# Kernel optimization log

Hardware: AMD Instinct MI355X
Metric: run time of the kernel (lower is better)

The kernel has to match this reference:

```python
import jax, jax.numpy as jnp
import numpy as np

B, S, D, H, L, M, V = 4, 4096, 512, 8, 6, 2048, 32000
C, NB, NBEF = 64, 64, 1      # chunk_len, n_buckets, n_chunks_before
DH = D // H


def sinusoid_pos_emb(seq_len, dim):
    pos = np.arange(seq_len, dtype=np.float32)[:, None]
    half = dim // 2
    freq = np.exp(np.arange(half, dtype=np.float32) * -(np.log(10000.0) / (half - 1)))
    pe = np.concatenate([np.sin(pos * freq), np.cos(pos * freq)], axis=-1)
    return jnp.asarray(pe, jnp.float32)  # [S, D]

POS = sinusoid_pos_emb(S, D)


def layer_norm(x, s, b):
    m = x.mean(-1, keepdims=True)
    v = ((x - m) ** 2).mean(-1, keepdims=True)
    return (x - m) * jax.lax.rsqrt(v + 1e-6) * s + b


def lsh_attention(x, Wq, Wv, Wo, rot, pad):
    """Shared-QK LSH bucketed chunked attention (Reformer, n_hashes=1, non-causal)."""
    q = jnp.einsum('bsd,dhf->bhsf', x, Wq.reshape(D, H, DH))
    v = jnp.einsum('bsd,dhf->bhsf', x, Wv.reshape(D, H, DH))
    # random-rotation hashing: bucket = argmax over [rot, -rot] projections
    r = jnp.einsum('bhsf,hfr->bhsr', q, rot)            # [B,H,S,NB//2]
    buckets = jnp.argmax(jnp.concatenate([r, -r], -1), -1)  # [B,H,S] in [0,NB)
    # stable sort by (bucket, position)
    st = jnp.argsort(buckets * S + jnp.arange(S), axis=-1)  # [B,H,S]
    g = lambda t: jnp.take_along_axis(t, st[..., None], axis=2)
    sq = g(q)
    sv = g(v)
    sk = sq  # shared QK (qk_length_norm=False)
    spad = jnp.take_along_axis(jnp.broadcast_to(pad[:, None, :], (B, H, S)), st, axis=2)
    nc = S // C
    cq = sq.reshape(B, H, nc, C, DH)
    ck = sk.reshape(B, H, nc, C, DH)
    cv = sv.reshape(B, H, nc, C, DH)
    cp = spad.reshape(B, H, nc, C)
    # look back NBEF chunks (wrap-around, as in trax look_adjacent)
    look = lambda t: jnp.concatenate([t] + [jnp.roll(t, i, axis=2) for i in range(1, NBEF + 1)], axis=3)
    bk, bv, bp = look(ck), look(cv), look(cp)   # keys of length C*(1+NBEF)
    logits = jnp.einsum('bhncf,bhnkf->bhnck', cq, bk) / jnp.sqrt(jnp.float32(DH))
    logits = jnp.where(bp[:, :, :, None, :], logits, -1e9)  # mask padded keys
    w = jax.nn.softmax(logits, axis=-1)
    o = jnp.einsum('bhnck,bhnkf->bhncf', w, bv).reshape(B, H, S, DH)
    # unsort back to original token order
    inv = jnp.argsort(st, axis=-1)
    o = jnp.take_along_axis(o, inv[..., None], axis=2)
    o = o.transpose(0, 2, 1, 3).reshape(B, S, D)
    return o @ Wo


def reference(tokens, emb, rot, ln1_s, ln1_b, Wq, Wv, Wo, ln2_s, ln2_b, W1, b1, W2, b2, lnf_s, lnf_b):
    pad = tokens > 0                     # [B,S] padding mask
    x = emb[tokens] + POS[None, :, :]    # embed + sinusoidal pos enc
    for l in range(L):
        h = layer_norm(x, ln1_s[l], ln1_b[l])
        x = x + lsh_attention(h, Wq[l], Wv[l], Wo[l], rot[l], pad)
        h = layer_norm(x, ln2_s[l], ln2_b[l])
        h = jax.nn.gelu(h @ W1[l] + b1[l]) @ W2[l] + b2[l]
        x = x + h
    return layer_norm(x, lnf_s, lnf_b)


def setup_inputs():
    key = jax.random.key(0)
    ks = jax.random.split(key, 8)
    w02 = lambda k, sh: jax.random.normal(k, sh, jnp.float32) * 0.02
    return dict(
        tokens=jax.random.randint(ks[0], (B, S), 1, V, dtype=jnp.int32),
        emb=jax.random.normal(ks[1], (V, D), jnp.float32),
        rot=jax.random.normal(ks[2], (L, H, DH, NB // 2), jnp.float32),
        ln1_s=jnp.ones((L, D)), ln1_b=jnp.zeros((L, D)),
        Wq=w02(ks[3], (L, D, D)), Wv=w02(ks[4], (L, D, D)), Wo=w02(ks[5], (L, D, D)),
        ln2_s=jnp.ones((L, D)), ln2_b=jnp.zeros((L, D)),
        W1=w02(ks[6], (L, D, M)), b1=jnp.zeros((L, M)),
        W2=w02(ks[7], (L, M, D)), b2=jnp.zeros((L, D)),
        lnf_s=jnp.ones((D,)), lnf_b=jnp.zeros((D,)),
    )
```

## Files before the change

kernel.cpp:

```cpp
#include <hip/hip_runtime.h>

#define B_ 4
#define S_ 4096
#define D_ 512
#define H_ 8
#define L_ 6
#define M_ 2048
#define DH_ 64
#define NC_ 64
#define C_ 64

typedef _Float16 half8 __attribute__((ext_vector_type(8)));
typedef _Float16 half4 __attribute__((ext_vector_type(4)));
typedef float f32x4 __attribute__((ext_vector_type(4)));

typedef const __attribute__((address_space(1))) unsigned int gu32;
typedef __attribute__((address_space(3))) unsigned int lu32;

#define OQ_ 0
#define OV_ 262144
#define OR_ 524288
#define OO_ 655360
#define O1_ 917504
#define O2_ 1966080
#define WTOT_ 3014656

__global__ __launch_bounds__(128) void embed_kernel(const int* __restrict__ tokens,
                                                    const float* __restrict__ emb,
                                                    float* __restrict__ x) {
  int row = blockIdx.x;
  int s = row & (S_ - 1);
  int tok = tokens[row];
  const float4* e = (const float4*)(emb + (size_t)tok * D_);
  float4* xo = (float4*)(x + (size_t)row * D_);
  int t = threadIdx.x;
  float4 ev = e[t];
  int d0 = t * 4;
  const double c64 = -9.210340371976184 / 255.0;
  float pe[4];
#pragma unroll
  for (int j = 0; j < 4; j++) {
    int d = d0 + j;
    int i = (d < 256) ? d : d - 256;
    double freq = exp((double)i * c64);
    double arg = (double)s * freq;
    pe[j] = (d < 256) ? (float)sin(arg) : (float)cos(arg);
  }
  float4 o;
  o.x = ev.x + pe[0];
  o.y = ev.y + pe[1];
  o.z = ev.z + pe[2];
  o.w = ev.w + pe[3];
  xo[t] = o;
}

__device__ __forceinline__ void ln_core(const float* __restrict__ in, int row, int t,
                                        const float* __restrict__ sc,
                                        const float* __restrict__ bi,
                                        float4& o1, float4& o2) {
  const float4* ir = (const float4*)(in + (size_t)row * D_);
  float4 a = ir[t];
  float4 b4 = ir[t + 64];
  float sum = a.x + a.y + a.z + a.w + b4.x + b4.y + b4.z + b4.w;
  float sq  = a.x*a.x + a.y*a.y + a.z*a.z + a.w*a.w
            + b4.x*b4.x + b4.y*b4.y + b4.z*b4.z + b4.w*b4.w;
#pragma unroll
  for (int m = 1; m < 64; m <<= 1) {
    sum += __shfl_xor(sum, m);
    sq  += __shfl_xor(sq, m);
  }
  float mean = sum * (1.0f / 512.0f);
  float var  = sq * (1.0f / 512.0f) - mean * mean;
  float rstd = 1.0f / sqrtf(var + 1e-6f);
  float4 s1 = ((const float4*)sc)[t], s2 = ((const float4*)sc)[t + 64];
  float4 g1 = ((const float4*)bi)[t], g2 = ((const float4*)bi)[t + 64];
  o1.x = (a.x - mean) * rstd * s1.x + g1.x;
  o1.y = (a.y - mean) * rstd * s1.y + g1.y;
  o1.z = (a.z - mean) * rstd * s1.z + g1.z;
  o1.w = (a.w - mean) * rstd * s1.w + g1.w;
  o2.x = (b4.x - mean) * rstd * s2.x + g2.x;
  o2.y = (b4.y - mean) * rstd * s2.y + g2.y;
  o2.z = (b4.z - mean) * rstd * s2.z + g2.z;
  o2.w = (b4.w - mean) * rstd * s2.w + g2.w;
}

__global__ __launch_bounds__(256) void ln_h(const float* __restrict__ in,
                                            _Float16* __restrict__ hi,
                                            _Float16* __restrict__ lo,
                                            const float* __restrict__ sc,
                                            const float* __restrict__ bi) {
  int row = blockIdx.x * 4 + (threadIdx.x >> 6);
  int t = threadIdx.x & 63;
  float4 o1, o2;
  ln_core(in, row, t, sc, bi, o1, o2);
  float v1[4] = {o1.x, o1.y, o1.z, o1.w};
  float v2[4] = {o2.x, o2.y, o2.z, o2.w};
  half4 h1, l1, h2, l2;
#pragma unroll
  for (int j = 0; j < 4; j++) {
    _Float16 h = (_Float16)v1[j];
    h1[j] = h; l1[j] = (_Float16)(v1[j] - (float)h);
    _Float16 g = (_Float16)v2[j];
    h2[j] = g; l2[j] = (_Float16)(v2[j] - (float)g);
  }
  size_t base = (size_t)row * D_;
  *(half4*)&hi[base + t * 4] = h1;
  *(half4*)&hi[base + 256 + t * 4] = h2;
  *(half4*)&lo[base + t * 4] = l1;
  *(half4*)&lo[base + 256 + t * 4] = l2;
}

__global__ __launch_bounds__(256) void ln_f(const float* __restrict__ in,
                                            float* __restrict__ out,
                                            const float* __restrict__ sc,
                                            const float* __restrict__ bi) {
  int row = blockIdx.x * 4 + (threadIdx.x >> 6);
  int t = threadIdx.x & 63;
  float4 o1, o2;
  ln_core(in, row, t, sc, bi, o1, o2);
  float4* orow = (float4*)(out + (size_t)row * D_);
  orow[t] = o1;
  orow[t + 64] = o2;
}

__device__ __forceinline__ float gelu_f(float v) {
  float v3 = v * v * v;
  return 0.5f * v * (1.0f + tanhf(0.7978845608028654f * (v + 0.044715f * v3)));
}

__device__ __forceinline__ void transp_tile(const float* __restrict__ src,
                                            _Float16* __restrict__ dhi,
                                            _Float16* __restrict__ dlo,
                                            int K, int N, int n0, int k0,
                                            float (*tile)[33]) {
  int tx = threadIdx.x & 31, ty = threadIdx.x >> 5;
#pragma unroll
  for (int i = 0; i < 4; i++)
    tile[ty + 8 * i][tx] = src[(size_t)(k0 + ty + 8 * i) * N + n0 + tx];
  __syncthreads();
#pragma unroll
  for (int i = 0; i < 4; i++) {
    int n = n0 + ty + 8 * i;
    float v = tile[tx][ty + 8 * i];
    _Float16 h = (_Float16)v;
    dhi[(size_t)n * K + k0 + tx] = h;
    dlo[(size_t)n * K + k0 + tx] = (_Float16)(v - (float)h);
  }
}

__global__ __launch_bounds__(256) void transp_cvt(const float* __restrict__ src,
                                                  _Float16* __restrict__ dhi,
                                                  _Float16* __restrict__ dlo,
                                                  int K, int N) {
  __shared__ float tile[32][33];
  transp_tile(src, dhi, dlo, K, N, blockIdx.x * 32, blockIdx.y * 32, tile);
}

__global__ __launch_bounds__(256) void transp_all(const float* __restrict__ Wq,
                                                  const float* __restrict__ Wv,
                                                  const float* __restrict__ Wo,
                                                  const float* __restrict__ W1,
                                                  const float* __restrict__ W2,
                                                  _Float16* __restrict__ whi,
                                                  _Float16* __restrict__ wlo) {
  __shared__ float tile[32][33];
  int bid = blockIdx.x;
  const float* src; _Float16 *dhi, *dlo; int K, N, t;
  if (bid < 256)       { src = Wq; dhi = whi + OQ_; dlo = wlo + OQ_; K = 512; N = 512;  t = bid; }
  else if (bid < 512)  { src = Wv; dhi = whi + OV_; dlo = wlo + OV_; K = 512; N = 512;  t = bid - 256; }
  else if (bid < 768)  { src = Wo; dhi = whi + OO_; dlo = wlo + OO_; K = 512; N = 512;  t = bid - 512; }
  else if (bid < 1792) { src = W1; dhi = whi + O1_; dlo = wlo + O1_; K = 512; N = 2048; t = bid - 768; }
  else                 { src = W2; dhi = whi + O2_; dlo = wlo + O2_; K = 2048; N = 512; t = bid - 1792; }
  int nx = N / 32;
  int n0 = (t % nx) * 32, k0 = (t / nx) * 32;
  transp_tile(src, dhi, dlo, K, N, n0, k0, tile);
}

template <int HAS_BIAS, int RESID, int DO_GELU, int OUT_HALF>
__global__ __launch_bounds__(256) void gemm_h(const _Float16* __restrict__ Ahi,
                                              const _Float16* __restrict__ Alo,
                                              const _Float16* __restrict__ Bhi,
                                              const _Float16* __restrict__ Blo,
                                              const float* __restrict__ bias,
                                              float* __restrict__ C,
                                              _Float16* __restrict__ Chi,
                                              _Float16* __restrict__ Clo,
                                              int M, int N, int K, int lda, int ldb) {
  __shared__ _Float16 lds[2][4][128 * 32];
  int tid = threadIdx.x;
  int nwg = gridDim.x * gridDim.y;
  int flat = blockIdx.y * gridDim.x + blockIdx.x;
  int chunk = nwg >> 3;
  int nf = (flat & 7) * chunk + (flat >> 3);
  int bx = nf % gridDim.x, by = nf / gridDim.x;
  int row0 = by * 128, col0 = bx * 128;
  int lane = tid & 63, w = tid >> 6;
  int wm = w >> 1, wn = w & 1;
  int fr = lane & 15, fk = (lane >> 4) * 8;
  int q4 = (lane >> 4) * 4;

  int sld = (w < 2) ? lda : ldb;
  int sbase = (w < 2) ? row0 : col0;
  const _Float16* plane = (w == 0) ? Ahi : (w == 1) ? Alo : (w == 2) ? Bhi : Blo;
  int scol = ((lane & 3) ^ ((lane >> 3) & 3)) * 8;
  const _Float16* gsrc = plane + (size_t)(sbase + (lane >> 2)) * sld + scol;
  size_t rowstep = (size_t)16 * sld;

  f32x4 acc[4][4];
#pragma unroll
  for (int m = 0; m < 4; m++)
#pragma unroll
    for (int n = 0; n < 4; n++) acc[m][n] = (f32x4){0.f, 0.f, 0.f, 0.f};

  int nst = K >> 5;
#pragma unroll
  for (int i = 0; i < 8; i++) {
    __builtin_amdgcn_global_load_lds((gu32*)(gsrc + (size_t)i * rowstep),
                                     (lu32*)&lds[0][w][i * 512], 16, 0, 0);
  }
  __syncthreads();

  int cur = 0;
  for (int s = 0; s < nst; ++s) {
    if (s + 1 < nst) {
      const _Float16* g = gsrc + (size_t)(s + 1) * 32;
#pragma unroll
      for (int i = 0; i < 8; i++) {
        __builtin_amdgcn_global_load_lds((gu32*)(g + (size_t)i * rowstep),
                                         (lu32*)&lds[cur ^ 1][w][i * 512], 16, 0, 0);
      }
    }
    const _Float16* Ah_ = lds[cur][0];
    const _Float16* Al_ = lds[cur][1];
    const _Float16* Bh_ = lds[cur][2];
    const _Float16* Bl_ = lds[cur][3];
    half8 bhf[4], blf[4];
#pragma unroll
    for (int n = 0; n < 4; n++) {
      int col = wn * 64 + n * 16 + fr;
      int fks = fk ^ (((col >> 1) & 3) << 3);
      bhf[n] = *(const half8*)&Bh_[col * 32 + fks];
      blf[n] = *(const half8*)&Bl_[col * 32 + fks];
    }
#pragma unroll
    for (int m = 0; m < 4; m++) {
      int row = wm * 64 + m * 16 + fr;
      int fks = fk ^ (((row >> 1) & 3) << 3);
      half8 ah = *(const half8*)&Ah_[row * 32 + fks];
      half8 al = *(const half8*)&Al_[row * 32 + fks];
#pragma unroll
      for (int n = 0; n < 4; n++)
        acc[m][n] = __builtin_amdgcn_mfma_f32_16x16x32_f16(bhf[n], ah, acc[m][n], 0, 0, 0);
#pragma unroll
      for (int n = 0; n < 4; n++)
        acc[m][n] = __builtin_amdgcn_mfma_f32_16x16x32_f16(bhf[n], al, acc[m][n], 0, 0, 0);
#pragma unroll
      for (int n = 0; n < 4; n++)
        acc[m][n] = __builtin_amdgcn_mfma_f32_16x16x32_f16(blf[n], ah, acc[m][n], 0, 0, 0);
    }
    __syncthreads();
    cur ^= 1;
  }

#pragma unroll
  for (int m = 0; m < 4; m++) {
    int row = row0 + wm * 64 + m * 16 + fr;
#pragma unroll
    for (int n = 0; n < 4; n++) {
      int colb = col0 + wn * 64 + n * 16 + q4;
      float4 bq = {0.f, 0.f, 0.f, 0.f};
      if (HAS_BIAS) bq = *(const float4*)&bias[colb];
      float v[4];
      v[0] = acc[m][n][0] + bq.x;
      v[1] = acc[m][n][1] + bq.y;
      v[2] = acc[m][n][2] + bq.z;
      v[3] = acc[m][n][3] + bq.w;
      if (DO_GELU) {
        v[0] = gelu_f(v[0]); v[1] = gelu_f(v[1]);
        v[2] = gelu_f(v[2]); v[3] = gelu_f(v[3]);
      }
      size_t idx = (size_t)row * N + colb;
      if (OUT_HALF) {
        half4 hv, lv;
#pragma unroll
        for (int r = 0; r < 4; r++) {
          _Float16 h = (_Float16)v[r];
          hv[r] = h;
          lv[r] = (_Float16)(v[r] - (float)h);
        }
        *(half4*)&Chi[idx] = hv;
        *(half4*)&Clo[idx] = lv;
      } else {
        float4 vv;
        vv.x = v[0]; vv.y = v[1]; vv.z = v[2]; vv.w = v[3];
        if (RESID) {
          float4 old = *(const float4*)&C[idx];
          vv.x += old.x; vv.y += old.y; vv.z += old.z; vv.w += old.w;
        }
        *(float4*)&C[idx] = vv;
      }
    }
  }
}

__global__ __launch_bounds__(256) void rotw_kernel(const float* __restrict__ Wq,
                                                   const float* __restrict__ rot,
                                                   float* __restrict__ rotW2) {
  int idx = blockIdx.x * 256 + threadIdx.x;
  int n = idx & 255;
  int d = idx >> 8;
  int h = n >> 5;
  int j = n & 31;
  double a = 0.0;
#pragma unroll 8
  for (int f = 0; f < 64; f++) {
    a += (double)Wq[(size_t)d * D_ + h * 64 + f] * (double)rot[((size_t)h * 64 + f) * 32 + j];
  }
  rotW2[idx] = (float)a;
}

__global__ __launch_bounds__(256) void argmax_kernel(const _Float16* __restrict__ qvr_hi,
                                                     const _Float16* __restrict__ qvr_lo,
                                                     int* __restrict__ buckets) {
  int gid = blockIdx.x * 256 + threadIdx.x;
  int s = gid & (S_ - 1);
  int bh = gid >> 12;
  int h = bh & (H_ - 1);
  int b = bh >> 3;
  size_t base = ((size_t)b * S_ + s) * 1280 + 1024 + h * 32;
  float r[32];
#pragma unroll
  for (int j8 = 0; j8 < 4; j8++) {
    half8 hv = *(const half8*)&qvr_hi[base + j8 * 8];
    half8 lv = *(const half8*)&qvr_lo[base + j8 * 8];
#pragma unroll
    for (int e = 0; e < 8; e++)
      r[j8 * 8 + e] = (float)hv[e] + (float)lv[e];
  }
  float best = r[0];
  int bi = 0;
#pragma unroll
  for (int j = 1; j < 64; j++) {
    float val = (j < 32) ? r[j] : -r[j - 32];
    if (val > best) { best = val; bi = j; }
  }
  buckets[gid] = bi;
}

__global__ __launch_bounds__(64) void sort_kernel(const int* __restrict__ buckets,
                                                  int* __restrict__ st) {
  __shared__ int hist[64][64];
  __shared__ int boff[64];
  int bh = blockIdx.x;
  const int* bk = buckets + (size_t)bh * S_;
  int* stb = st + (size_t)bh * S_;
  int t = threadIdx.x;
  for (int j = 0; j < 64; j++) hist[t][j] = 0;
  __syncthreads();
  for (int i = 0; i < 64; i++) {
    int s = t * 64 + i;
    hist[t][bk[s]]++;
  }
  __syncthreads();
  int run = 0;
  for (int tt = 0; tt < 64; tt++) {
    int c = hist[tt][t];
    hist[tt][t] = run;
    run += c;
  }
  boff[t] = run;
  __syncthreads();
  if (t == 0) {
    int acc = 0;
    for (int j = 0; j < 64; j++) { int c = boff[j]; boff[j] = acc; acc += c; }
  }
  __syncthreads();
  for (int i = 0; i < 64; i++) {
    int s = t * 64 + i;
    int bkt = bk[s];
    int pos = boff[bkt] + hist[t][bkt];
    hist[t][bkt] = hist[t][bkt] + 1;
    stb[pos] = s;
  }
}

#define KP 72
#define VP 136
__global__ __launch_bounds__(256) void attn_mfma(const _Float16* __restrict__ qvhi,
                                                 const _Float16* __restrict__ qvlo,
                                                 const int* __restrict__ st,
                                                 _Float16* __restrict__ ohi,
                                                 _Float16* __restrict__ olo) {
  __shared__ _Float16 lds[35840];
  const int KH = 0, KL = 9216, VH = 18432, VL = 27136;
  int blk = blockIdx.x;
  int n = blk & (NC_ - 1);
  int bh = blk >> 6;
  int h = bh & (H_ - 1);
  int b = bh >> 3;
  const int* stbh = st + (size_t)bh * S_;
  int tid = threadIdx.x;
  int pn = (n + NC_ - 1) & (NC_ - 1);

  {
    int r = tid >> 1, dseg = (tid & 1) * 32;
    int si = (r < 64) ? (n * 64 + r) : (pn * 64 + (r - 64));
    int p = stbh[si];
    size_t gb = ((size_t)b * S_ + p) * 1280 + h * 64 + dseg;
    half8 kh[4], kl[4], vh8[4], vl8[4];
#pragma unroll
    for (int j = 0; j < 4; j++) {
      kh[j] = *(const half8*)&qvhi[gb + j * 8];
      kl[j] = *(const half8*)&qvlo[gb + j * 8];
      vh8[j] = *(const half8*)&qvhi[gb + 512 + j * 8];
      vl8[j] = *(const half8*)&qvlo[gb + 512 + j * 8];
    }
#pragma unroll
    for (int j = 0; j < 4; j++) {
      *(half8*)&lds[KH + r * KP + dseg + j * 8] = kh[j];
      *(half8*)&lds[KL + r * KP + dseg + j * 8] = kl[j];
    }
#pragma unroll
    for (int j = 0; j < 4; j++) {
#pragma unroll
      for (int e = 0; e < 8; e++) {
        int dim = dseg + j * 8 + e;
        lds[VH + dim * VP + r] = vh8[j][e];
        lds[VL + dim * VP + r] = vl8[j][e];
      }
    }
  }
  __syncthreads();

  int lane = tid & 63, w = tid >> 6;
  int fr = lane & 15, fk8 = (lane >> 4) * 8;
  int q4 = (lane >> 4) * 4;

  int qrow = w * 16 + fr;
  half8 qh0 = *(half8*)&lds[KH + qrow * KP + fk8];
  half8 qh1 = *(half8*)&lds[KH + qrow * KP + 32 + fk8];
  half8 ql0 = *(half8*)&lds[KL + qrow * KP + fk8];
  half8 ql1 = *(half8*)&lds[KL + qrow * KP + 32 + fk8];

  f32x4 sa[8];
#pragma unroll
  for (int nc = 0; nc < 8; nc++) {
    int key = nc * 16 + fr;
    half8 bh0 = *(half8*)&lds[KH + key * KP + fk8];
    half8 bh1 = *(half8*)&lds[KH + key * KP + 32 + fk8];
    half8 bl0 = *(half8*)&lds[KL + key * KP + fk8];
    half8 bl1 = *(half8*)&lds[KL + key * KP + 32 + fk8];
    f32x4 a = (f32x4){0.f, 0.f, 0.f, 0.f};
    a = __builtin_amdgcn_mfma_f32_16x16x32_f16(qh0, bh0, a, 0, 0, 0);
    a = __builtin_amdgcn_mfma_f32_16x16x32_f16(qh1, bh1, a, 0, 0, 0);
    a = __builtin_amdgcn_mfma_f32_16x16x32_f16(ql0, bh0, a, 0, 0, 0);
    a = __builtin_amdgcn_mfma_f32_16x16x32_f16(ql1, bh1, a, 0, 0, 0);
    a = __builtin_amdgcn_mfma_f32_16x16x32_f16(qh0, bl0, a, 0, 0, 0);
    a = __builtin_amdgcn_mfma_f32_16x16x32_f16(qh1, bl1, a, 0, 0, 0);
    sa[nc] = a;
  }

  float inv[4];
#pragma unroll
  for (int reg = 0; reg < 4; reg++) {
    float m = sa[0][reg];
#pragma unroll
    for (int nc = 1; nc < 8; nc++) m = fmaxf(m, sa[nc][reg]);
    m = fmaxf(m, __shfl_xor(m, 1));
    m = fmaxf(m, __shfl_xor(m, 2));
    m = fmaxf(m, __shfl_xor(m, 4));
    m = fmaxf(m, __shfl_xor(m, 8));
    float s = 0.f;
#pragma unroll
    for (int nc = 0; nc < 8; nc++) {
      float e = expf(0.125f * (sa[nc][reg] - m));
      sa[nc][reg] = e;
      s += e;
    }
    s += __shfl_xor(s, 1);
    s += __shfl_xor(s, 2);
    s += __shfl_xor(s, 4);
    s += __shfl_xor(s, 8);
    inv[reg] = 1.0f / s;
  }

  __syncthreads();

  int PW = w * 4352;
#pragma unroll
  for (int nc = 0; nc < 8; nc++) {
#pragma unroll
    for (int reg = 0; reg < 4; reg++) {
      float pv = sa[nc][reg] * inv[reg];
      _Float16 ph = (_Float16)pv;
      _Float16 pl = (_Float16)(pv - (float)ph);
      int prow = (lane >> 4) * 4 + reg;
      int key = nc * 16 + fr;
      lds[PW + prow * VP + key] = ph;
      lds[PW + 2176 + prow * VP + key] = pl;
    }
  }

  half8 ph8[4], pl8[4];
#pragma unroll
  for (int kt = 0; kt < 4; kt++) {
    ph8[kt] = *(half8*)&lds[PW + fr * VP + kt * 32 + fk8];
    pl8[kt] = *(half8*)&lds[PW + 2176 + fr * VP + kt * 32 + fk8];
  }
  f32x4 oa[4];
#pragma unroll
  for (int nco = 0; nco < 4; nco++) {
    int dim = nco * 16 + fr;
    f32x4 a = (f32x4){0.f, 0.f, 0.f, 0.f};
#pragma unroll
    for (int kt = 0; kt < 4; kt++) {
      half8 bvh = *(half8*)&lds[VH + dim * VP + kt * 32 + fk8];
      half8 bvl = *(half8*)&lds[VL + dim * VP + kt * 32 + fk8];
      a = __builtin_amdgcn_mfma_f32_16x16x32_f16(bvh, ph8[kt], a, 0, 0, 0);
      a = __builtin_amdgcn_mfma_f32_16x16x32_f16(bvh, pl8[kt], a, 0, 0, 0);
      a = __builtin_amdgcn_mfma_f32_16x16x32_f16(bvl, ph8[kt], a, 0, 0, 0);
    }
    oa[nco] = a;
  }

  {
    int qq = w * 16 + fr;
    int p = stbh[n * 64 + qq];
    size_t ob = ((size_t)b * S_ + p) * D_ + h * 64;
#pragma unroll
    for (int nco = 0; nco < 4; nco++) {
      half4 hv, lv;
#pragma unroll
      for (int r = 0; r < 4; r++) {
        float val = oa[nco][r];
        _Float16 h16 = (_Float16)val;
        hv[r] = h16;
        lv[r] = (_Float16)(val - (float)h16);
      }
      *(half4*)&ohi[ob + nco * 16 + q4] = hv;
      *(half4*)&olo[ob + nco * 16 + q4] = lv;
    }
  }
}

extern "C" void kernel_launch(void* const* d_in, const int* in_sizes, int n_in,
                              void* d_out, int out_size, void* d_ws, size_t ws_size,
                              hipStream_t stream) {
  const int*   tokens = (const int*)d_in[0];
  const float* emb    = (const float*)d_in[1];
  const float* rot    = (const float*)d_in[2];
  const float* ln1_s  = (const float*)d_in[3];
  const float* ln1_b  = (const float*)d_in[4];
  const float* Wq     = (const float*)d_in[5];
  const float* Wv     = (const float*)d_in[6];
  const float* Wo     = (const float*)d_in[7];
  const float* ln2_s  = (const float*)d_in[8];
  const float* ln2_b  = (const float*)d_in[9];
  const float* W1     = (const float*)d_in[10];
  const float* b1     = (const float*)d_in[11];
  const float* W2     = (const float*)d_in[12];
  const float* b2     = (const float*)d_in[13];
  const float* lnf_s  = (const float*)d_in[14];
  const float* lnf_b  = (const float*)d_in[15];

  float* x = (float*)d_out;
  const size_t RS = (size_t)B_ * S_ * D_;
  const size_t WTOT = WTOT_;

  char* wsb = (char*)d_ws;
  const int rows = B_ * S_;
  _Float16* qvr_hi = (_Float16*)wsb;
  _Float16* qvr_lo = qvr_hi + (size_t)rows * 1280;
  _Float16* obuf_hi = (_Float16*)(wsb + 2 * (size_t)rows * 1280 * 2);
  _Float16* obuf_lo = obuf_hi + RS;
  _Float16* mid_hi = (_Float16*)wsb;
  _Float16* mid_lo = (_Float16*)(wsb + 4 * RS);
  _Float16* hbuf_hi = (_Float16*)(wsb + 14 * RS);
  _Float16* hbuf_lo = (_Float16*)(wsb + 16 * RS);
  _Float16* whi = (_Float16*)(wsb + 18 * RS);
  _Float16* wlo = whi + WTOT;
  float* rotW2 = (float*)(wlo + WTOT);
  int* buckets = (int*)(rotW2 + 512 * 256);
  int* stbuf   = buckets + B_ * H_ * S_;

  const int Mh = M_ / 2;

  embed_kernel<<<rows, 128, 0, stream>>>(tokens, emb, x);

  for (int l = 0; l < L_; l++) {
    transp_all<<<2816, 256, 0, stream>>>(Wq + (size_t)l * D_ * D_, Wv + (size_t)l * D_ * D_,
                                         Wo + (size_t)l * D_ * D_, W1 + (size_t)l * D_ * M_,
                                         W2 + (size_t)l * M_ * D_, whi, wlo);
    rotw_kernel<<<(D_ * 256) / 256, 256, 0, stream>>>(Wq + (size_t)l * D_ * D_,
                                                      rot + (size_t)l * H_ * DH_ * 32, rotW2);
    transp_cvt<<<dim3(256 / 32, D_ / 32), 256, 0, stream>>>(rotW2, whi + OR_, wlo + OR_, D_, 256);

    ln_h<<<rows / 4, 256, 0, stream>>>(x, hbuf_hi, hbuf_lo, ln1_s + (size_t)l * D_, ln1_b + (size_t)l * D_);

    dim3 gqv(1280 / 128, rows / 128);
    gemm_h<0, 0, 0, 1><<<gqv, 256, 0, stream>>>(hbuf_hi, hbuf_lo, whi + OQ_, wlo + OQ_, nullptr,
                                                nullptr, qvr_hi, qvr_lo, rows, 1280, D_, D_, D_);

    argmax_kernel<<<(B_ * H_ * S_) / 256, 256, 0, stream>>>(qvr_hi, qvr_lo, buckets);
    sort_kernel<<<B_ * H_, 64, 0, stream>>>(buckets, stbuf);
    attn_mfma<<<B_ * H_ * NC_, 256, 0, stream>>>(qvr_hi, qvr_lo, stbuf, obuf_hi, obuf_lo);

    dim3 g1(D_ / 128, rows / 128);
    gemm_h<0, 1, 0, 0><<<g1, 256, 0, stream>>>(obuf_hi, obuf_lo, whi + OO_, wlo + OO_, nullptr,
                                               x, nullptr, nullptr, rows, D_, D_, D_, D_);

    ln_h<<<rows / 4, 256, 0, stream>>>(x, hbuf_hi, hbuf_lo, ln2_s + (size_t)l * D_, ln2_b + (size_t)l * D_);

    for (int ch = 0; ch < 2; ch++) {
      dim3 gf1(Mh / 128, rows / 128);
      gemm_h<1, 0, 1, 1><<<gf1, 256, 0, stream>>>(hbuf_hi, hbuf_lo,
                                                  whi + O1_ + (size_t)ch * Mh * D_,
                                                  wlo + O1_ + (size_t)ch * Mh * D_,
                                                  b1 + (size_t)l * M_ + ch * Mh,
                                                  nullptr, mid_hi, mid_lo, rows, Mh, D_, D_, D_);
      dim3 gf2(D_ / 128, rows / 128);
      if (ch == 0) {
        gemm_h<0, 1, 0, 0><<<gf2, 256, 0, stream>>>(mid_hi, mid_lo,
                                                    whi + O2_,
                                                    wlo + O2_,
                                                    nullptr, x, nullptr, nullptr,
                                                    rows, D_, Mh, Mh, M_);
      } else {
        gemm_h<1, 1, 0, 0><<<gf2, 256, 0, stream>>>(mid_hi, mid_lo,
                                                    whi + O2_ + (size_t)ch * Mh,
                                                    wlo + O2_ + (size_t)ch * Mh,
                                                    b2 + (size_t)l * D_, x, nullptr, nullptr,
                                                    rows, D_, Mh, Mh, M_);
      }
    }
  }

  ln_f<<<rows / 4, 256, 0, stream>>>(x, x, lnf_s, lnf_b);
}
```

Measured before the change: 2.856 ms.

## Use 128x64 GEMM tiles with triple-buffered LDS pipeline and MFMA priority

Shrinks the GEMM output tile from 128x128 to 128x64 and doubles the grid width, so more workgroups are available to spread across the CUs. The LDS pipeline goes from double to triple buffering: each thread issues 6 async global-to-LDS loads, and the code uses explicit vmcnt waits plus a single barrier per K step instead of two syncthreads. s_setprio is raised around the MFMA block. The trade-off is less data reuse per tile and more redundant A-tile loads, in exchange for better occupancy and deeper latency hiding.

```diff
diff --git a/kernel.cpp b/kernel.cpp
--- a/kernel.cpp
+++ b/kernel.cpp
@@ -186,62 +186,78 @@
                                               _Float16* __restrict__ Chi,
                                               _Float16* __restrict__ Clo,
                                               int M, int N, int K, int lda, int ldb) {
-  __shared__ _Float16 lds[2][4][128 * 32];
+  __shared__ _Float16 lds[3][12288];
   int tid = threadIdx.x;
   int nwg = gridDim.x * gridDim.y;
   int flat = blockIdx.y * gridDim.x + blockIdx.x;
   int chunk = nwg >> 3;
   int nf = (flat & 7) * chunk + (flat >> 3);
   int bx = nf % gridDim.x, by = nf / gridDim.x;
-  int row0 = by * 128, col0 = bx * 128;
+  int row0 = by * 128, col0 = bx * 64;
   int lane = tid & 63, w = tid >> 6;
   int wm = w >> 1, wn = w & 1;
   int fr = lane & 15, fk = (lane >> 4) * 8;
   int q4 = (lane >> 4) * 4;
 
-  int sld = (w < 2) ? lda : ldb;
-  int sbase = (w < 2) ? row0 : col0;
-  const _Float16* plane = (w == 0) ? Ahi : (w == 1) ? Alo : (w == 2) ? Bhi : Blo;
+  const _Float16* srcs[6];
+  unsigned ldsof[6];
   int scol = ((lane & 3) ^ ((lane >> 3) & 3)) * 8;
-  const _Float16* gsrc = plane + (size_t)(sbase + (lane >> 2)) * sld + scol;
-  size_t rowstep = (size_t)16 * sld;
-
-  f32x4 acc[4][4];
+#pragma unroll
+  for (int i = 0; i < 6; i++) {
+    int c = w * 6 + i;
+    const _Float16* pb;
+    int ld, base, prow;
+    unsigned poff;
+    if (c < 8)       { pb = Ahi; ld = lda; base = row0; prow = c * 16;        poff = 0u; }
+    else if (c < 16) { pb = Alo; ld = lda; base = row0; prow = (c - 8) * 16;  poff = 4096u; }
+    else if (c < 20) { pb = Bhi; ld = ldb; base = col0; prow = (c - 16) * 16; poff = 8192u; }
+    else             { pb = Blo; ld = ldb; base = col0; prow = (c - 20) * 16; poff = 10240u; }
+    srcs[i] = pb + (size_t)(base + prow + (lane >> 2)) * ld + scol;
+    ldsof[i] = poff + (unsigned)prow * 32u;
+  }
+
+  f32x4 acc[4][2];
 #pragma unroll
   for (int m = 0; m < 4; m++)
 #pragma unroll
-    for (int n = 0; n < 4; n++) acc[m][n] = (f32x4){0.f, 0.f, 0.f, 0.f};
+    for (int n = 0; n < 2; n++) acc[m][n] = (f32x4){0.f, 0.f, 0.f, 0.f};
 
   int nst = K >> 5;
 #pragma unroll
-  for (int i = 0; i < 8; i++) {
-    __builtin_amdgcn_global_load_lds((gu32*)(gsrc + (size_t)i * rowstep),
-                                     (lu32*)&lds[0][w][i * 512], 16, 0, 0);
-  }
-  __syncthreads();
-
-  int cur = 0;
-  for (int s = 0; s < nst; ++s) {
-    if (s + 1 < nst) {
-      const _Float16* g = gsrc + (size_t)(s + 1) * 32;
-#pragma unroll
-      for (int i = 0; i < 8; i++) {
-        __builtin_amdgcn_global_load_lds((gu32*)(g + (size_t)i * rowstep),
-                                         (lu32*)&lds[cur ^ 1][w][i * 512], 16, 0, 0);
-      }
-    }
-    const _Float16* Ah_ = lds[cur][0];
-    const _Float16* Al_ = lds[cur][1];
-    const _Float16* Bh_ = lds[cur][2];
-    const _Float16* Bl_ = lds[cur][3];
-    half8 bhf[4], blf[4];
-#pragma unroll
-    for (int n = 0; n < 4; n++) {
-      int col = wn * 64 + n * 16 + fr;
+  for (int i = 0; i < 6; i++)
+    __builtin_amdgcn_global_load_lds((gu32*)srcs[i], (lu32*)&lds[0][ldsof[i]], 16, 0, 0);
+#pragma unroll
+  for (int i = 0; i < 6; i++)
+    __builtin_amdgcn_global_load_lds((gu32*)(srcs[i] + 32), (lu32*)&lds[1][ldsof[i]], 16, 0, 0);
+
+  int ir = 0;
+  for (int t = 0; t < nst; ++t) {
+    if (t + 1 < nst) {
+      asm volatile("s_waitcnt vmcnt(6)" ::: "memory");
+    } else {
+      asm volatile("s_waitcnt vmcnt(0)" ::: "memory");
+    }
+    __builtin_amdgcn_s_barrier();
+    if (t + 2 < nst) {
+      int ib = ir + 2; if (ib >= 3) ib -= 3;
+      int off = (t + 2) * 32;
+#pragma unroll
+      for (int i = 0; i < 6; i++)
+        __builtin_amdgcn_global_load_lds((gu32*)(srcs[i] + off), (lu32*)&lds[ib][ldsof[i]], 16, 0, 0);
+    }
+    const _Float16* Ah_ = &lds[ir][0];
+    const _Float16* Al_ = &lds[ir][4096];
+    const _Float16* Bh_ = &lds[ir][8192];
+    const _Float16* Bl_ = &lds[ir][10240];
+    half8 bhf[2], blf[2];
+#pragma unroll
+    for (int n = 0; n < 2; n++) {
+      int col = wn * 32 + n * 16 + fr;
       int fks = fk ^ (((col >> 1) & 3) << 3);
       bhf[n] = *(const half8*)&Bh_[col * 32 + fks];
       blf[n] = *(const half8*)&Bl_[col * 32 + fks];
     }
+    __builtin_amdgcn_s_setprio(1);
 #pragma unroll
     for (int m = 0; m < 4; m++) {
       int row = wm * 64 + m * 16 + fr;
@@ -249,25 +265,25 @@
       half8 ah = *(const half8*)&Ah_[row * 32 + fks];
       half8 al = *(const half8*)&Al_[row * 32 + fks];
 #pragma unroll
-      for (int n = 0; n < 4; n++)
+      for (int n = 0; n < 2; n++)
         acc[m][n] = __builtin_amdgcn_mfma_f32_16x16x32_f16(bhf[n], ah, acc[m][n], 0, 0, 0);
 #pragma unroll
-      for (int n = 0; n < 4; n++)
+      for (int n = 0; n < 2; n++)
         acc[m][n] = __builtin_amdgcn_mfma_f32_16x16x32_f16(bhf[n], al, acc[m][n], 0, 0, 0);
 #pragma unroll
-      for (int n = 0; n < 4; n++)
+      for (int n = 0; n < 2; n++)
         acc[m][n] = __builtin_amdgcn_mfma_f32_16x16x32_f16(blf[n], ah, acc[m][n], 0, 0, 0);
     }
-    __syncthreads();
-    cur ^= 1;
+    __builtin_amdgcn_s_setprio(0);
+    ir = ir + 1; if (ir >= 3) ir -= 3;
   }
 
 #pragma unroll
   for (int m = 0; m < 4; m++) {
     int row = row0 + wm * 64 + m * 16 + fr;
 #pragma unroll
-    for (int n = 0; n < 4; n++) {
-      int colb = col0 + wn * 64 + n * 16 + q4;
+    for (int n = 0; n < 2; n++) {
+      int colb = col0 + wn * 32 + n * 16 + q4;
       float4 bq = {0.f, 0.f, 0.f, 0.f};
       if (HAS_BIAS) bq = *(const float4*)&bias[colb];
       float v[4];
@@ -597,7 +613,7 @@
 
     ln_h<<<rows / 4, 256, 0, stream>>>(x, hbuf_hi, hbuf_lo, ln1_s + (size_t)l * D_, ln1_b + (size_t)l * D_);
 
-    dim3 gqv(1280 / 128, rows / 128);
+    dim3 gqv(1280 / 64, rows / 128);
     gemm_h<0, 0, 0, 1><<<gqv, 256, 0, stream>>>(hbuf_hi, hbuf_lo, whi + OQ_, wlo + OQ_, nullptr,
                                                 nullptr, qvr_hi, qvr_lo, rows, 1280, D_, D_, D_);
 
@@ -605,20 +621,20 @@
     sort_kernel<<<B_ * H_, 64, 0, stream>>>(buckets, stbuf);
     attn_mfma<<<B_ * H_ * NC_, 256, 0, stream>>>(qvr_hi, qvr_lo, stbuf, obuf_hi, obuf_lo);
 
-    dim3 g1(D_ / 128, rows / 128);
+    dim3 g1(D_ / 64, rows / 128);
     gemm_h<0, 1, 0, 0><<<g1, 256, 0, stream>>>(obuf_hi, obuf_lo, whi + OO_, wlo + OO_, nullptr,
                                                x, nullptr, nullptr, rows, D_, D_, D_, D_);
 
     ln_h<<<rows / 4, 256, 0, stream>>>(x, hbuf_hi, hbuf_lo, ln2_s + (size_t)l * D_, ln2_b + (size_t)l * D_);
 
     for (int ch = 0; ch < 2; ch++) {
-      dim3 gf1(Mh / 128, rows / 128);
+      dim3 gf1(Mh / 64, rows / 128);
       gemm_h<1, 0, 1, 1><<<gf1, 256, 0, stream>>>(hbuf_hi, hbuf_lo,
                                                   whi + O1_ + (size_t)ch * Mh * D_,
                                                   wlo + O1_ + (size_t)ch * Mh * D_,
                                                   b1 + (size_t)l * M_ + ch * Mh,
                                                   nullptr, mid_hi, mid_lo, rows, Mh, D_, D_, D_);
-      dim3 gf2(D_ / 128, rows / 128);
+      dim3 gf2(D_ / 64, rows / 128);
       if (ch == 0) {
         gemm_h<0, 1, 0, 0><<<gf2, 256, 0, stream>>>(mid_hi, mid_lo,
                                                     whi + O2_,
```

New measurement: 3.175 ms. 11.2% more time.
